# Kernel optimization log

Measured on AMD Instinct MI355X. Metric: run time of the kernel, lower is better.

## Reference

```python
import jax, jax.numpy as jnp
from jax import lax
import numpy as np

POINT_PAIRS = 10000
SIGMA = 0.03
ALPHA = 1.0
MIN_DEPTH = -0.001
MAX_DEPTH = 80.0


def _get_edges(images):
    # images: [n,3,H,W]; Sobel on channel 0, VALID conv then zero-pad by 1 (as in torch code)
    x = images[:, :1]
    kx = jnp.array([[-1., 0., 1.], [-2., 0., 2.], [-1., 0., 1.]], jnp.float32).reshape(1, 1, 3, 3)
    ky = jnp.array([[1., 2., 1.], [0., 0., 0.], [-1., -2., -1.]], jnp.float32).reshape(1, 1, 3, 3)
    gx = lax.conv_general_dilated(x, kx, (1, 1), 'VALID')
    gy = lax.conv_general_dilated(x, ky, (1, 1), 'VALID')
    edges = jnp.sqrt(gx * gx + gy * gy)
    thetas = jnp.arctan2(gy, gx)
    pad = ((0, 0), (0, 0), (1, 1), (1, 1))
    return jnp.pad(edges, pad), jnp.pad(thetas, pad)


def _sample_and_loss(key, inp, tgt, edge, theta, smask):
    # inp/tgt/edge/theta: [H,W] float; smask: [H,W] bool
    H, W = inp.shape
    k1, k2, k3 = jax.random.split(key, 3)
    # edge-guided anchor sampling: uniform over {edge >= 0.1*max} & strict_mask, with replacement
    emask = (edge >= 0.1 * edge.max()) & smask
    p = emask.reshape(-1).astype(jnp.float32)
    p = p / jnp.maximum(p.sum(), 1.0)
    flat_idx = jax.random.choice(k1, H * W, (POINT_PAIRS,), replace=True, p=p)
    sh = flat_idx // W
    sw = flat_idx % W
    th = theta.reshape(-1)[flat_idx]
    # signed step distances along / perpendicular to the edge direction
    dist = jax.random.randint(k2, (4, POINT_PAIRS), 2, 31).astype(jnp.float32)
    sign = jnp.array([-1., -1., 1., 1.], jnp.float32).reshape(4, 1)
    dist = dist * sign
    # random_direct: p<0.5 -> along gradient; else rotate theta by pi/2 (swapped cos/sin)
    pdir = jax.random.uniform(k3) < 0.5
    th2 = ((th + jnp.pi / 2) + jnp.pi) % (2 * jnp.pi) - jnp.pi
    col1 = sw[None, :] + jnp.round(dist * jnp.cos(th)[None, :]).astype(jnp.int32)
    row1 = sh[None, :] + jnp.round(dist * jnp.sin(th)[None, :]).astype(jnp.int32)
    col2 = sw[None, :] + jnp.round(dist * jnp.sin(th2)[None, :]).astype(jnp.int32)
    row2 = sh[None, :] + jnp.round(dist * jnp.cos(th2)[None, :]).astype(jnp.int32)
    col = jnp.where(pdir, col1, col2)  # [4,N]
    row = jnp.where(pdir, row1, row2)
    inb = (col >= 0) & (col <= W - 1) & (row >= 0) & (row <= H - 1)
    valid = jnp.all(inb, axis=0)  # [N]; torch drops these columns, we mask instead
    colc = jnp.clip(col, 0, W - 1)
    rowc = jnp.clip(row, 0, H - 1)
    # pairs (a,b),(b,c),(c,d) -> A = [a,b,c], B = [b,c,d]
    rA = jnp.concatenate([rowc[0], rowc[1], rowc[2]])
    cA = jnp.concatenate([colc[0], colc[1], colc[2]])
    rB = jnp.concatenate([rowc[1], rowc[2], rowc[3]])
    cB = jnp.concatenate([colc[1], colc[2], colc[3]])
    vm = jnp.concatenate([valid, valid, valid]).astype(jnp.float32)  # [3N]
    iA = inp[rA, cA]
    iB = inp[rB, cB]
    tA = tgt[rA, cA]
    tB = tgt[rB, cB]
    # ranking loss
    ratio = (tA + 1e-6) / (tB + 1e-6)
    absdiff = jnp.abs(tA - tB)
    maxdiff = jnp.max(jnp.where(vm > 0, absdiff, 0.0))
    tw = jnp.exp(absdiff / (maxdiff + 1e-6))
    eq = (ratio < 1.0 + SIGMA) & (ratio > 1.0 / (1.0 + SIGMA))
    labels = jnp.where(ratio >= 1.0 + SIGMA, 1.0,
                       jnp.where(ratio <= 1.0 / (1.0 + SIGMA), -1.0, 0.0))
    equal_loss = (iA - iB) ** 2 / tw * eq.astype(jnp.float32)
    unequal_loss = jnp.log1p(jnp.exp((iB - iA) * labels)) * (1.0 - eq.astype(jnp.float32))
    cnt = jnp.maximum(vm.sum(), 1.0)
    loss = ALPHA * jnp.sum(equal_loss * vm) / cnt + jnp.sum(unequal_loss * vm) / cnt
    return loss, vm.sum()


def setup_inputs() -> dict:
    key = jax.random.key(0)
    k1, k2, k3, k4 = jax.random.split(key, 4)
    n, H, W = 8, 1024, 1024
    inputs = jax.random.normal(k1, (n, 1, H, W), jnp.float32)
    targets = jax.random.uniform(k2, (n, 1, H, W), jnp.float32)
    images = jax.random.uniform(k3, (n, 3, H, W), jnp.float32)
    depth_gt = jax.random.uniform(k4, (n, 1, H, W), jnp.float32)
    return {"inputs": inputs, "targets": targets, "images": images, "depth_gt": depth_gt}


def reference(inputs, targets, images, depth_gt):
    n = inputs.shape[0]
    strict = (depth_gt > MIN_DEPTH) & (depth_gt < MAX_DEPTH) & ~(targets == 80.0)
    edges, thetas = _get_edges(images)
    keys = jax.random.split(jax.random.key(42), n)
    losses, counts = jax.vmap(_sample_and_loss)(
        keys, inputs[:, 0], targets[:, 0], edges[:, 0], thetas[:, 0], strict[:, 0])
    return losses.sum() / n, counts.sum() / n
```

## Files before the change

### kernel.cpp

```cpp
#include <hip/hip_runtime.h>
#include <math.h>
#include <stdint.h>

#define NIMG 8
#define HH 1024
#define WW 1024
#define NPIX (HH*WW)
#define PAIRS 10000
#define STRIP 8
#define NSTRIPS 128
#define S1BLOCKS 40
#define WSLOTS (S1BLOCKS*4)
#define FBLK 4
#define QPAIRS (PAIRS/FBLK)

#define OFF_EDGE 0
#define OFF_MD   1024
#define OFF_RES  4096
#define OFF_CTR  4352

__device__ __forceinline__ uint64_t mix64(uint64_t x){
    x += 0x9E3779B97F4A7C15ull;
    x = (x ^ (x >> 30)) * 0xBF58476D1CE4E5B9ull;
    x = (x ^ (x >> 27)) * 0x94D049BB133111EBull;
    return x ^ (x >> 31);
}

__device__ __forceinline__ float block_reduce_max(float v, float* sm){
    for (int off = 32; off; off >>= 1)
        v = fmaxf(v, __shfl_down(v, off));
    int wv = threadIdx.x >> 6, lane = threadIdx.x & 63;
    if (lane == 0) sm[wv] = v;
    __syncthreads();
    if (threadIdx.x == 0)
        sm[0] = fmaxf(fmaxf(sm[0], sm[1]), fmaxf(sm[2], sm[3]));
    __syncthreads();
    float r = sm[0];
    __syncthreads();
    return r;
}

__device__ __forceinline__ float block_reduce_sum(float v, float* sm){
    for (int off = 32; off; off >>= 1)
        v += __shfl_down(v, off);
    int wv = threadIdx.x >> 6, lane = threadIdx.x & 63;
    if (lane == 0) sm[wv] = v;
    __syncthreads();
    if (threadIdx.x == 0)
        sm[0] = sm[0] + sm[1] + sm[2] + sm[3];
    __syncthreads();
    float r = sm[0];
    __syncthreads();
    return r;
}

__device__ __forceinline__ void load16(const float* __restrict__ p, float* d){
    const float4* q = (const float4*)p;
    float4 v0 = q[0], v1 = q[1], v2 = q[2], v3 = q[3];
    d[0]=v0.x; d[1]=v0.y; d[2]=v0.z; d[3]=v0.w;
    d[4]=v1.x; d[5]=v1.y; d[6]=v1.z; d[7]=v1.w;
    d[8]=v2.x; d[9]=v2.y; d[10]=v2.z; d[11]=v2.w;
    d[12]=v3.x; d[13]=v3.y; d[14]=v3.z; d[15]=v3.w;
}

__global__ __launch_bounds__(256) void edgemax_kernel(const float* __restrict__ images,
                                                      float* __restrict__ ws){
    if (blockIdx.x == 0){
        ws[OFF_RES + threadIdx.x] = 0.0f;
        if (threadIdx.x == 0) ws[OFF_CTR] = 0.0f;
    }

    int img  = blockIdx.x & 7;
    int xb   = blockIdx.x >> 3;
    const float* x = images + (size_t)img * 3 * NPIX;
    int wv   = threadIdx.x >> 6;
    int lane = threadIdx.x & 63;
    int strip = xb * 4 + wv;
    int r0 = 1 + strip * STRIP;
    int r1 = min(r0 + STRIP - 1, HH - 2);
    int c0 = lane * 16;

    float a[16], b[16], n[16];
    load16(x + (size_t)(r0-1)*WW + c0, a);
    load16(x + (size_t)r0*WW + c0, b);

    float m = 0.0f;
    for (int r = r0; r <= r1; ++r){
        load16(x + (size_t)(r+1)*WW + c0, n);
        float sx[16], dy[16];
        #pragma unroll
        for (int i = 0; i < 16; ++i){
            sx[i] = a[i] + 2.0f*b[i] + n[i];
            dy[i] = a[i] - n[i];
        }
        float sxl = __shfl_up(sx[15], 1);
        float sxr = __shfl_down(sx[0], 1);
        float dyl = __shfl_up(dy[15], 1);
        float dyr = __shfl_down(dy[0], 1);
        #pragma unroll
        for (int j = 0; j < 16; ++j){
            float sl = (j == 0)  ? sxl : sx[j-1];
            float sr = (j == 15) ? sxr : sx[j+1];
            float dl = (j == 0)  ? dyl : dy[j-1];
            float dr = (j == 15) ? dyr : dy[j+1];
            float gx = sr - sl;
            float gy = dl + 2.0f*dy[j] + dr;
            float e2 = gx*gx + gy*gy;
            int c = c0 + j;
            if (c >= 1 && c <= WW-2) m = fmaxf(m, e2);
        }
        #pragma unroll
        for (int i = 0; i < 16; ++i){ a[i] = b[i]; b[i] = n[i]; }
    }
    for (int off = 32; off; off >>= 1)
        m = fmaxf(m, __shfl_down(m, off));
    if (lane == 0)
        ws[OFF_EDGE + img * NSTRIPS + strip] = m;
}

struct AttLd {
    int r, c, rl, cl;
    float a, b, cc, d, e, f, g, h, dg, tg;
};

__device__ __forceinline__ AttLd att_issue(uint64_t u,
        const float* __restrict__ x, const float* __restrict__ tgt,
        const float* __restrict__ dgt){
    AttLd s;
    uint32_t pix = (uint32_t)(u >> 44);
    s.r  = (int)(pix >> 10);
    s.c  = (int)(pix & (WW - 1));
    s.rl = min(max(s.r, 1), HH-2);
    s.cl = min(max(s.c, 1), WW-2);
    const float* p0 = x + (size_t)(s.rl-1)*WW + s.cl;
    const float* p1 = x + (size_t)s.rl*WW + s.cl;
    const float* p2 = x + (size_t)(s.rl+1)*WW + s.cl;
    s.a = p0[-1]; s.b = p0[0]; s.cc = p0[1];
    s.d = p1[-1];               s.e = p1[1];
    s.f = p2[-1]; s.g = p2[0];  s.h = p2[1];
    s.dg = dgt[s.rl*WW + s.cl];
    s.tg = tgt[s.rl*WW + s.cl];
    return s;
}

__global__ __launch_bounds__(256) void sample_kernel(
                               const float* __restrict__ inputs,
                               const float* __restrict__ targets,
                               const float* __restrict__ images,
                               const float* __restrict__ depth_gt,
                               float* __restrict__ ws,
                               float4* __restrict__ recsA,
                               float4* __restrict__ recsB){
    __shared__ float sred[4];
    int img = blockIdx.x & 7;
    int jb  = blockIdx.x >> 3;
    int tid = threadIdx.x;
    int j   = jb * 256 + tid;
    const float* x   = images   + (size_t)img * 3 * NPIX;
    const float* inp = inputs   + (size_t)img * NPIX;
    const float* tgt = targets  + (size_t)img * NPIX;
    const float* dgt = depth_gt + (size_t)img * NPIX;

    float ev = 0.0f;
    if (tid < NSTRIPS) ev = ws[OFF_EDGE + img * NSTRIPS + tid];
    float thr2 = 0.01f * block_reduce_max(ev, sred);

    float mdiff = 0.0f;
    float4 recA = make_float4(0.f, 0.f, 0.f, 0.f);
    float4 recB = make_float4(0.f, 0.f, 0.f, 0.f);

    if (j < PAIRS){
        uint64_t base = ((uint64_t)(img * PAIRS + j)) << 10;
        bool pdir = (mix64(((uint64_t)(NIMG * PAIRS + img)) << 10) & 1ull) != 0ull;

        int sh = -1, sw = -1;
        float gxs = 0.f, gys = 0.f, e2s = 1.f;

        AttLd cur = att_issue(mix64(base + 0ull), x, tgt, dgt);
        for (int att = 0; att < 900; ++att){
            AttLd nxt = att_issue(mix64(base + (uint64_t)(att + 1)), x, tgt, dgt);
            float gx = (cur.cc - cur.a) + 2.0f*(cur.e - cur.d) + (cur.h - cur.f);
            float gy = (cur.a + 2.0f*cur.b + cur.cc) - (cur.f + 2.0f*cur.g + cur.h);
            float e2 = gx*gx + gy*gy;
            bool pass = (cur.r == cur.rl) && (cur.c == cur.cl) && (e2 >= thr2) &&
                        (cur.dg > -0.001f && cur.dg < 80.0f) && (cur.tg != 80.0f);
            if (pass){
                sh = cur.rl; sw = cur.cl; gxs = gx; gys = gy; e2s = e2;
                break;
            }
            cur = nxt;
        }

        if (sh >= 0){
            float inv = rsqrtf(e2s);
            float cmul = gxs * inv;
            float rmul = gys * inv;
            if (!pdir) cmul = -cmul;

            uint64_t u0 = mix64(base + 1000ull);
            uint64_t u1 = mix64(base + 1001ull);
            float dist[4];
            dist[0] = -(float)(2u + (uint32_t)(u0 & 0xFFFFFFFFull) % 29u);
            dist[1] = -(float)(2u + (uint32_t)(u0 >> 32) % 29u);
            dist[2] =  (float)(2u + (uint32_t)(u1 & 0xFFFFFFFFull) % 29u);
            dist[3] =  (float)(2u + (uint32_t)(u1 >> 32) % 29u);

            int rowc[4], colc[4];
            bool valid = true;
            #pragma unroll
            for (int k = 0; k < 4; ++k){
                int cc2 = sw + (int)rintf(dist[k] * cmul);
                int rr2 = sh + (int)rintf(dist[k] * rmul);
                if (cc2 < 0 || cc2 > WW-1 || rr2 < 0 || rr2 > HH-1) valid = false;
                colc[k] = min(max(cc2, 0), WW-1);
                rowc[k] = min(max(rr2, 0), HH-1);
            }

            if (valid){
                float t4[4], i4[4];
                #pragma unroll
                for (int k = 0; k < 4; ++k){
                    int p = rowc[k]*WW + colc[k];
                    t4[k] = tgt[p];
                    i4[k] = inp[p];
                }
                float d2a[3], ada[3];
                float un = 0.0f;
                #pragma unroll
                for (int k = 0; k < 3; ++k){
                    float tA = t4[k], tB = t4[k+1];
                    float ratio = (tA + 1e-6f) / (tB + 1e-6f);
                    float adk = fabsf(tA - tB);
                    mdiff = fmaxf(mdiff, adk);
                    bool eq = (ratio < 1.03f) && (ratio > 0.9708737864077669f);
                    if (eq){
                        float d = i4[k] - i4[k+1];
                        d2a[k] = d*d; ada[k] = adk;
                    } else {
                        d2a[k] = 0.f; ada[k] = 0.f;
                        float lab = (ratio >= 1.03f) ? 1.0f : -1.0f;
                        un += log1pf(expf((i4[k+1] - i4[k]) * lab));
                    }
                }
                recA = make_float4(d2a[0], d2a[1], d2a[2], un);
                recB = make_float4(ada[0], ada[1], ada[2], 3.0f);
            }
        }
        recsA[img * PAIRS + j] = recA;
        recsB[img * PAIRS + j] = recB;
    }

    for (int off = 32; off; off >>= 1)
        mdiff = fmaxf(mdiff, __shfl_down(mdiff, off));
    if ((tid & 63) == 0)
        ws[OFF_MD + img * WSLOTS + jb*4 + (tid >> 6)] = mdiff;
}

__global__ __launch_bounds__(256) void finish_kernel(
                               float* __restrict__ ws,
                               const float4* __restrict__ recsA,
                               const float4* __restrict__ recsB,
                               float* __restrict__ out){
    __shared__ float sred[4];
    __shared__ unsigned lastflag;
    int img = blockIdx.x & 7;
    int q   = blockIdx.x >> 3;
    int tid = threadIdx.x;

    float mv = 0.0f;
    if (tid < WSLOTS) mv = ws[OFF_MD + img * WSLOTS + tid];
    float md = block_reduce_max(mv, sred);
    float inv = 1.0f / (md + 1e-6f);

    float loss = 0.0f, cnt = 0.0f;
    int base = img * PAIRS + q * QPAIRS;
    for (int r = tid; r < QPAIRS; r += 256){
        float4 A = recsA[base + r];
        float4 B = recsB[base + r];
        loss += A.w
              + A.x * expf(-B.x * inv)
              + A.y * expf(-B.y * inv)
              + A.z * expf(-B.z * inv);
        cnt  += B.w;
    }
    loss = block_reduce_sum(loss, sred);
    cnt  = block_reduce_sum(cnt, sred);

    if (tid == 0){
        atomicAdd(&ws[OFF_RES + img*32 + 0], loss);
        atomicAdd(&ws[OFF_RES + img*32 + 1], cnt);
        __threadfence();
        unsigned old = atomicAdd((unsigned int*)&ws[OFF_CTR], 1u);
        lastflag = (old == (unsigned)(NIMG*FBLK - 1)) ? 1u : 0u;
    }
    __syncthreads();

    if (lastflag){
        __threadfence();
        float val = 0.0f, cv = 0.0f;
        if (tid < NIMG){
            float li = atomicAdd(&ws[OFF_RES + tid*32 + 0], 0.0f);
            float ci = atomicAdd(&ws[OFF_RES + tid*32 + 1], 0.0f);
            val = li / fmaxf(ci, 1.0f);
            cv  = ci;
        }
        for (int off = 4; off; off >>= 1){
            val += __shfl_down(val, off);
            cv  += __shfl_down(cv,  off);
        }
        if (tid == 0){
            out[0] = val / (float)NIMG;
            out[1] = cv  / (float)NIMG;
        }
    }
}

extern "C" void kernel_launch(void* const* d_in, const int* in_sizes, int n_in,
                              void* d_out, int out_size, void* d_ws, size_t ws_size,
                              hipStream_t stream) {
    const float* inputs  = (const float*)d_in[0];
    const float* targets = (const float*)d_in[1];
    const float* images  = (const float*)d_in[2];
    const float* depth   = (const float*)d_in[3];
    float* out = (float*)d_out;

    float* ws     = (float*)d_ws;
    float4* recsA = (float4*)((char*)d_ws + 65536);
    float4* recsB = recsA + (size_t)NIMG * PAIRS;

    hipLaunchKernelGGL(edgemax_kernel, dim3(NSTRIPS/4 * NIMG), dim3(256), 0, stream,
                       images, ws);
    hipLaunchKernelGGL(sample_kernel, dim3(S1BLOCKS * NIMG), dim3(256), 0, stream,
                       inputs, targets, images, depth, ws, recsA, recsB);
    hipLaunchKernelGGL(finish_kernel, dim3(NIMG * FBLK), dim3(256), 0, stream,
                       ws, recsA, recsB, out);
}
```

Measured before the change: 38.20 us.

## Split each point pair across four lanes and pre-reduce unequal loss per wave

The sample kernel now gives each of the four sampled points of a pair its own thread, so the grid is four times larger. Pair validity is combined with a wave ballot, and neighbouring point values are exchanged with shuffles. The unequal-loss term and the pair count are summed per wave and written to the workspace, so the finish kernel only reads compact float2 records for the equal-loss term. The aim is better occupancy and latency hiding on the dependent gather and sampling loops. In exchange, all four threads of a pair repeat the rejection-sampling loop.

```diff
diff --git a/kernel.cpp b/kernel.cpp
--- a/kernel.cpp
+++ b/kernel.cpp
@@ -9,15 +9,18 @@
 #define PAIRS 10000
 #define STRIP 8
 #define NSTRIPS 128
-#define S1BLOCKS 40
-#define WSLOTS (S1BLOCKS*4)
+#define SBLK 160
+#define PSTRIDE 640
 #define FBLK 4
-#define QPAIRS (PAIRS/FBLK)
+#define QREC (PAIRS*4/FBLK)
+#define QSLOT (PSTRIDE/FBLK)
 
 #define OFF_EDGE 0
 #define OFF_MD   1024
-#define OFF_RES  4096
-#define OFF_CTR  4352
+#define OFF_UN   6144
+#define OFF_CNT  11264
+#define OFF_RES  16384
+#define OFF_CTR  16640
 
 __device__ __forceinline__ uint64_t mix64(uint64_t x){
     x += 0x9E3779B97F4A7C15ull;
@@ -66,8 +69,8 @@
 __global__ __launch_bounds__(256) void edgemax_kernel(const float* __restrict__ images,
                                                       float* __restrict__ ws){
     if (blockIdx.x == 0){
-        ws[OFF_RES + threadIdx.x] = 0.0f;
-        if (threadIdx.x == 0) ws[OFF_CTR] = 0.0f;
+        for (int i = threadIdx.x; i < 288; i += 256)
+            ws[OFF_RES + i] = 0.0f;
     }
 
     int img  = blockIdx.x & 7;
@@ -149,13 +152,16 @@
                                const float* __restrict__ images,
                                const float* __restrict__ depth_gt,
                                float* __restrict__ ws,
-                               float4* __restrict__ recsA,
-                               float4* __restrict__ recsB){
+                               float2* __restrict__ recs){
     __shared__ float sred[4];
-    int img = blockIdx.x & 7;
-    int jb  = blockIdx.x >> 3;
-    int tid = threadIdx.x;
-    int j   = jb * 256 + tid;
+    int img  = blockIdx.x & 7;
+    int jb   = blockIdx.x >> 3;
+    int tid  = threadIdx.x;
+    int lane = tid & 63;
+    int grpb = lane & ~3;
+    int g    = jb * 256 + tid;
+    int j    = g >> 2;
+    int sub  = g & 3;
     const float* x   = images   + (size_t)img * 3 * NPIX;
     const float* inp = inputs   + (size_t)img * NPIX;
     const float* tgt = targets  + (size_t)img * NPIX;
@@ -165,9 +171,8 @@
     if (tid < NSTRIPS) ev = ws[OFF_EDGE + img * NSTRIPS + tid];
     float thr2 = 0.01f * block_reduce_max(ev, sred);
 
-    float mdiff = 0.0f;
-    float4 recA = make_float4(0.f, 0.f, 0.f, 0.f);
-    float4 recB = make_float4(0.f, 0.f, 0.f, 0.f);
+    float mdiff = 0.0f, un = 0.0f, cntv = 0.0f;
+    float d2 = 0.0f, ad = 0.0f;
 
     if (j < PAIRS){
         uint64_t base = ((uint64_t)(img * PAIRS + j)) << 10;
@@ -191,75 +196,67 @@
             cur = nxt;
         }
 
+        bool inb = false;
+        float tA = 0.f, iA = 0.f;
         if (sh >= 0){
             float inv = rsqrtf(e2s);
             float cmul = gxs * inv;
             float rmul = gys * inv;
             if (!pdir) cmul = -cmul;
 
-            uint64_t u0 = mix64(base + 1000ull);
-            uint64_t u1 = mix64(base + 1001ull);
-            float dist[4];
-            dist[0] = -(float)(2u + (uint32_t)(u0 & 0xFFFFFFFFull) % 29u);
-            dist[1] = -(float)(2u + (uint32_t)(u0 >> 32) % 29u);
-            dist[2] =  (float)(2u + (uint32_t)(u1 & 0xFFFFFFFFull) % 29u);
-            dist[3] =  (float)(2u + (uint32_t)(u1 >> 32) % 29u);
-
-            int rowc[4], colc[4];
-            bool valid = true;
-            #pragma unroll
-            for (int k = 0; k < 4; ++k){
-                int cc2 = sw + (int)rintf(dist[k] * cmul);
-                int rr2 = sh + (int)rintf(dist[k] * rmul);
-                if (cc2 < 0 || cc2 > WW-1 || rr2 < 0 || rr2 > HH-1) valid = false;
-                colc[k] = min(max(cc2, 0), WW-1);
-                rowc[k] = min(max(rr2, 0), HH-1);
+            uint64_t uu = mix64(base + 1000ull + (uint64_t)(sub >> 1));
+            uint32_t half = (sub & 1) ? (uint32_t)(uu >> 32)
+                                      : (uint32_t)(uu & 0xFFFFFFFFull);
+            float dist = (float)(2u + half % 29u) * ((sub < 2) ? -1.0f : 1.0f);
+
+            int cc2 = sw + (int)rintf(dist * cmul);
+            int rr2 = sh + (int)rintf(dist * rmul);
+            inb = (cc2 >= 0 && cc2 <= WW-1 && rr2 >= 0 && rr2 <= HH-1);
+            int p = min(max(rr2, 0), HH-1)*WW + min(max(cc2, 0), WW-1);
+            tA = tgt[p];
+            iA = inp[p];
+        }
+        unsigned long long vb = __ballot((sh >= 0) && inb);
+        bool valid = (sh >= 0) && (((vb >> grpb) & 0xFull) == 0xFull);
+
+        float tB = __shfl_down(tA, 1);
+        float iB = __shfl_down(iA, 1);
+
+        if (valid && sub < 3){
+            float ratio = (tA + 1e-6f) / (tB + 1e-6f);
+            float adk = fabsf(tA - tB);
+            mdiff = adk;
+            bool eq = (ratio < 1.03f) && (ratio > 0.9708737864077669f);
+            if (eq){
+                float d = iA - iB;
+                d2 = d*d; ad = adk;
+            } else {
+                float lab = (ratio >= 1.03f) ? 1.0f : -1.0f;
+                un = log1pf(expf((iB - iA) * lab));
             }
-
-            if (valid){
-                float t4[4], i4[4];
-                #pragma unroll
-                for (int k = 0; k < 4; ++k){
-                    int p = rowc[k]*WW + colc[k];
-                    t4[k] = tgt[p];
-                    i4[k] = inp[p];
-                }
-                float d2a[3], ada[3];
-                float un = 0.0f;
-                #pragma unroll
-                for (int k = 0; k < 3; ++k){
-                    float tA = t4[k], tB = t4[k+1];
-                    float ratio = (tA + 1e-6f) / (tB + 1e-6f);
-                    float adk = fabsf(tA - tB);
-                    mdiff = fmaxf(mdiff, adk);
-                    bool eq = (ratio < 1.03f) && (ratio > 0.9708737864077669f);
-                    if (eq){
-                        float d = i4[k] - i4[k+1];
-                        d2a[k] = d*d; ada[k] = adk;
-                    } else {
-                        d2a[k] = 0.f; ada[k] = 0.f;
-                        float lab = (ratio >= 1.03f) ? 1.0f : -1.0f;
-                        un += log1pf(expf((i4[k+1] - i4[k]) * lab));
-                    }
-                }
-                recA = make_float4(d2a[0], d2a[1], d2a[2], un);
-                recB = make_float4(ada[0], ada[1], ada[2], 3.0f);
-            }
-        }
-        recsA[img * PAIRS + j] = recA;
-        recsB[img * PAIRS + j] = recB;
-    }
-
-    for (int off = 32; off; off >>= 1)
-        mdiff = fmaxf(mdiff, __shfl_down(mdiff, off));
-    if ((tid & 63) == 0)
-        ws[OFF_MD + img * WSLOTS + jb*4 + (tid >> 6)] = mdiff;
+        }
+        if (valid && sub == 0) cntv = 3.0f;
+
+        recs[(size_t)img * PAIRS * 4 + g] = make_float2(d2, ad);
+    }
+
+    float m_ = mdiff, u_ = un, c_ = cntv;
+    for (int off = 32; off; off >>= 1){
+        m_ = fmaxf(m_, __shfl_down(m_, off));
+        u_ += __shfl_down(u_, off);
+        c_ += __shfl_down(c_, off);
+    }
+    if (lane == 0){
+        int slot = jb*4 + (tid >> 6);
+        ws[OFF_MD  + img * PSTRIDE + slot] = m_;
+        ws[OFF_UN  + img * PSTRIDE + slot] = u_;
+        ws[OFF_CNT + img * PSTRIDE + slot] = c_;
+    }
 }
 
 __global__ __launch_bounds__(256) void finish_kernel(
                                float* __restrict__ ws,
-                               const float4* __restrict__ recsA,
-                               const float4* __restrict__ recsB,
+                               const float2* __restrict__ recs,
                                float* __restrict__ out){
     __shared__ float sred[4];
     __shared__ unsigned lastflag;
@@ -268,23 +265,25 @@
     int tid = threadIdx.x;
 
     float mv = 0.0f;
-    if (tid < WSLOTS) mv = ws[OFF_MD + img * WSLOTS + tid];
+    for (int s = tid; s < PSTRIDE; s += 256)
+        mv = fmaxf(mv, ws[OFF_MD + img * PSTRIDE + s]);
     float md = block_reduce_max(mv, sred);
     float inv = 1.0f / (md + 1e-6f);
 
-    float loss = 0.0f, cnt = 0.0f;
-    int base = img * PAIRS + q * QPAIRS;
-    for (int r = tid; r < QPAIRS; r += 256){
-        float4 A = recsA[base + r];
-        float4 B = recsB[base + r];
-        loss += A.w
-              + A.x * expf(-B.x * inv)
-              + A.y * expf(-B.y * inv)
-              + A.z * expf(-B.z * inv);
-        cnt  += B.w;
-    }
-    loss = block_reduce_sum(loss, sred);
-    cnt  = block_reduce_sum(cnt, sred);
+    float uv = 0.0f, cv = 0.0f;
+    for (int s = q*QSLOT + tid; s < (q+1)*QSLOT; s += 256){
+        uv += ws[OFF_UN  + img * PSTRIDE + s];
+        cv += ws[OFF_CNT + img * PSTRIDE + s];
+    }
+
+    float eqs = 0.0f;
+    const float2* sp = recs + (size_t)img * PAIRS * 4 + (size_t)q * QREC;
+    for (int r = tid; r < QREC; r += 256){
+        float2 s = sp[r];
+        eqs += s.x * expf(-s.y * inv);
+    }
+    float loss = block_reduce_sum(eqs + uv, sred);
+    float cnt  = block_reduce_sum(cv, sred);
 
     if (tid == 0){
         atomicAdd(&ws[OFF_RES + img*32 + 0], loss);
@@ -297,20 +296,20 @@
 
     if (lastflag){
         __threadfence();
-        float val = 0.0f, cv = 0.0f;
+        float val = 0.0f, cv2 = 0.0f;
         if (tid < NIMG){
             float li = atomicAdd(&ws[OFF_RES + tid*32 + 0], 0.0f);
             float ci = atomicAdd(&ws[OFF_RES + tid*32 + 1], 0.0f);
             val = li / fmaxf(ci, 1.0f);
-            cv  = ci;
+            cv2 = ci;
         }
         for (int off = 4; off; off >>= 1){
             val += __shfl_down(val, off);
-            cv  += __shfl_down(cv,  off);
+            cv2 += __shfl_down(cv2, off);
         }
         if (tid == 0){
             out[0] = val / (float)NIMG;
-            out[1] = cv  / (float)NIMG;
+            out[1] = cv2 / (float)NIMG;
         }
     }
 }
@@ -324,14 +323,13 @@
     const float* depth   = (const float*)d_in[3];
     float* out = (float*)d_out;
 
-    float* ws     = (float*)d_ws;
-    float4* recsA = (float4*)((char*)d_ws + 65536);
-    float4* recsB = recsA + (size_t)NIMG * PAIRS;
+    float* ws    = (float*)d_ws;
+    float2* recs = (float2*)((char*)d_ws + 131072);
 
     hipLaunchKernelGGL(edgemax_kernel, dim3(NSTRIPS/4 * NIMG), dim3(256), 0, stream,
                        images, ws);
-    hipLaunchKernelGGL(sample_kernel, dim3(S1BLOCKS * NIMG), dim3(256), 0, stream,
-                       inputs, targets, images, depth, ws, recsA, recsB);
+    hipLaunchKernelGGL(sample_kernel, dim3(SBLK * NIMG), dim3(256), 0, stream,
+                       inputs, targets, images, depth, ws, recs);
     hipLaunchKernelGGL(finish_kernel, dim3(NIMG * FBLK), dim3(256), 0, stream,
-                       ws, recsA, recsB, out);
-}
+                       ws, recs, out);
+}
```

Result: slower. 46.03 us (+20.5%).
